# Kernel tuning notes

Hardware: AMD Instinct MI355X
Metric: run time of the kernel (lower is better)

The kernel has to match this reference:

```python
import jax, jax.numpy as jnp
import numpy as np

EPS = 1e-7  # keras.backend.epsilon()


def setup_inputs() -> dict:
    key = jax.random.key(0)
    kx, kw, ku = jax.random.split(key, 3)
    B, S, F = 16, 4096, 512
    x = jax.random.normal(kx, (B, S, F), dtype=jnp.float32)
    # glorot-uniform-scaled weights
    limW = np.sqrt(6.0 / (F + F)).astype(np.float32)
    W = jax.random.uniform(kw, (F, F), dtype=jnp.float32, minval=-limW, maxval=limW)
    b = jnp.zeros((F,), dtype=jnp.float32)
    limu = np.sqrt(6.0 / (F + 1)).astype(np.float32)
    u = jax.random.uniform(ku, (F,), dtype=jnp.float32, minval=-limu, maxval=limu)
    return {"x": x, "W": W, "b": b, "u": u}


def reference(x, W, b, u):
    # x: [B,S,F]  W: [F,F]  b: [F]  u: [F]
    h = jnp.tanh(jnp.einsum('bsf,fg->bsg', x, W) + b)   # [B,S,F]
    scores = jnp.einsum('bsf,f->bs', h, u)              # [B,S]
    e = jnp.exp(scores)
    # NOTE: faithful to the source, normalization is GLOBAL over all B*S scores
    a = e / (jnp.sum(e) + EPS)                          # [B,S]
    out = jnp.einsum('bsf,bs->bf', x, a)                # [B,F] weighted-sum pool over steps
    return out
```

## Files before the change

### kernel.cpp

```cpp
#include <hip/hip_runtime.h>
#include <stdint.h>

#define EPSV 1e-7f
#define FDIM 512
#define BK 64
#define NROWS 65536

typedef __bf16 bf16_t;
typedef bf16_t bf16x8 __attribute__((ext_vector_type(8)));
typedef unsigned short ushort8 __attribute__((ext_vector_type(8)));
typedef float f32x4 __attribute__((ext_vector_type(4)));

#define AS1 __attribute__((address_space(1)))
#define AS3 __attribute__((address_space(3)))

__device__ __forceinline__ unsigned short f2bf(float f) {
  union { float f; unsigned int u; } c; c.f = f;
  unsigned int u = c.u;
  unsigned int r = u + 0x7fffu + ((u >> 16) & 1u);
  return (unsigned short)(r >> 16);
}

__device__ __forceinline__ float fast_tanh(float x) {
  x = fminf(15.0f, fmaxf(-15.0f, x));
  float t = __expf(2.0f * x);
  return 1.0f - 2.0f * __builtin_amdgcn_rcpf(t + 1.0f);
}

__global__ void convert_W(const float* __restrict__ W, unsigned short* __restrict__ Wt) {
  __shared__ unsigned short tile[32][34];
  const int t = threadIdx.x;
  const int tx = t & 31, ty = t >> 5;
  const int bn = blockIdx.x & 15, bk = blockIdx.x >> 4;
  const int k0 = bk * 32, n0 = bn * 32;
#pragma unroll
  for (int i = 0; i < 4; ++i) {
    int r = ty + i * 8;
    tile[r][tx] = f2bf(W[(size_t)(k0 + r) * FDIM + n0 + tx]);
  }
  __syncthreads();
#pragma unroll
  for (int i = 0; i < 4; ++i) {
    int r = ty + i * 8;
    Wt[(size_t)(n0 + r) * FDIM + k0 + tx] = tile[tx][r];
  }
}

__global__ __launch_bounds__(256, 4) void gemm_score(
    const float* __restrict__ x, const unsigned short* __restrict__ Wt,
    const float* __restrict__ bvec, const float* __restrict__ uvec,
    float* __restrict__ spart) {
  __shared__ unsigned short sA[128 * BK];
  __shared__ unsigned short sB[128 * BK];
  __shared__ float score_s[128];
  __shared__ float ub_s[128], bb_s[128];

  const int t = threadIdx.x;
  const int lane = t & 63;
  const int w = t >> 6;
  const int wm = w & 1;
  const int wn = w >> 1;
  const int quad = lane >> 4;
  const int l15 = lane & 15;
  const int rt = blockIdx.x >> 2;
  const int nch = blockIdx.x & 3;
  const int m0 = rt * 128;
  const int col0 = nch * 128;

  if (t < 128) {
    score_s[t] = 0.0f;
    ub_s[t] = uvec[col0 + t];
    bb_s[t] = bvec[col0 + t];
  }

  f32x4 acc[4][4];
#pragma unroll
  for (int mi = 0; mi < 4; ++mi)
#pragma unroll
    for (int ni = 0; ni < 4; ++ni) acc[mi][ni] = (f32x4){0.f, 0.f, 0.f, 0.f};

  for (int kc = 0; kc < FDIM / BK; ++kc) {
    const int kbase = kc * BK;
#pragma unroll
    for (int p = 0; p < 4; ++p) {
      int slot = t + 256 * p;
      int row = slot >> 3;
      int j = (slot & 7) ^ (row & 7);
      const float* g = x + (size_t)(m0 + row) * FDIM + kbase + j * 8;
      float4 lo = *(const float4*)g;
      float4 hi = *(const float4*)(g + 4);
      ushort8 v;
      v[0] = f2bf(lo.x); v[1] = f2bf(lo.y); v[2] = f2bf(lo.z); v[3] = f2bf(lo.w);
      v[4] = f2bf(hi.x); v[5] = f2bf(hi.y); v[6] = f2bf(hi.z); v[7] = f2bf(hi.w);
      *(ushort8*)(void*)(sA + slot * 8) = v;
    }
#pragma unroll
    for (int i = 0; i < 4; ++i) {
      int nb = w * 32 + i * 8;
      int nl = nb + (lane >> 3);
      int j = (lane & 7) ^ (nl & 7);
      const unsigned short* g =
          Wt + (size_t)(col0 + nl) * FDIM + kbase + j * 8;
      unsigned short* l = (unsigned short*)(sB + nb * 64);
      __builtin_amdgcn_global_load_lds((AS1 void*)(g), (AS3 void*)(l), 16, 0, 0);
    }
    __syncthreads();
#pragma unroll
    for (int ks = 0; ks < 2; ++ks) {
      bf16x8 af[4], bfr[4];
#pragma unroll
      for (int mi = 0; mi < 4; ++mi) {
        int row = wm * 64 + mi * 16 + l15;
        int phys = (ks * 4 + quad) ^ (row & 7);
        af[mi] = *(const bf16x8*)(const void*)(sA + row * 64 + phys * 8);
      }
#pragma unroll
      for (int ni = 0; ni < 4; ++ni) {
        int row = wn * 64 + ni * 16 + l15;
        int phys = (ks * 4 + quad) ^ (row & 7);
        bfr[ni] = *(const bf16x8*)(const void*)(sB + row * 64 + phys * 8);
      }
#pragma unroll
      for (int mi = 0; mi < 4; ++mi)
#pragma unroll
        for (int ni = 0; ni < 4; ++ni)
          acc[mi][ni] = __builtin_amdgcn_mfma_f32_16x16x32_bf16(
              af[mi], bfr[ni], acc[mi][ni], 0, 0, 0);
    }
    __syncthreads();
  }

  float sc[4][4];
#pragma unroll
  for (int mi = 0; mi < 4; ++mi)
#pragma unroll
    for (int r = 0; r < 4; ++r) sc[mi][r] = 0.0f;
#pragma unroll
  for (int ni = 0; ni < 4; ++ni) {
    int cl = wn * 64 + ni * 16 + l15;
    float uu = ub_s[cl], bb = bb_s[cl];
#pragma unroll
    for (int mi = 0; mi < 4; ++mi)
#pragma unroll
      for (int r = 0; r < 4; ++r)
        sc[mi][r] += uu * fast_tanh(acc[mi][ni][r] + bb);
  }
#pragma unroll
  for (int mi = 0; mi < 4; ++mi)
#pragma unroll
    for (int r = 0; r < 4; ++r) {
      float v = sc[mi][r];
      v += __shfl_xor(v, 1); v += __shfl_xor(v, 2);
      v += __shfl_xor(v, 4); v += __shfl_xor(v, 8);
      if (l15 == 0)
        atomicAdd(&score_s[wm * 64 + mi * 16 + quad * 4 + r], v);
    }
  __syncthreads();
  if (t < 128) spart[(size_t)nch * NROWS + m0 + t] = score_s[t];
}

__global__ void score_exp(float* __restrict__ spart, float* __restrict__ sumE) {
  __shared__ float ws_[4];
  const int t = threadIdx.x;
  const int i = blockIdx.x * 256 + t;
  float s = spart[i] + spart[i + NROWS] + spart[i + 2 * NROWS] + spart[i + 3 * NROWS];
  float e = __expf(s);
  spart[i] = e;
  float v = e;
  v += __shfl_xor(v, 1);  v += __shfl_xor(v, 2);  v += __shfl_xor(v, 4);
  v += __shfl_xor(v, 8);  v += __shfl_xor(v, 16); v += __shfl_xor(v, 32);
  if ((t & 63) == 0) ws_[t >> 6] = v;
  __syncthreads();
  if (t == 0) atomicAdd(sumE, ws_[0] + ws_[1] + ws_[2] + ws_[3]);
}

__global__ __launch_bounds__(256) void pool_k(
    const float* __restrict__ x, const float* __restrict__ e,
    const float* __restrict__ sumE, float* __restrict__ out) {
  __shared__ float e_s[128];
  __shared__ float4 red[128];
  const int t = threadIdx.x;
  const int b = blockIdx.x >> 5, chunk = blockIdx.x & 31;
  const int g0 = b * 4096 + chunk * 128;
  if (t < 128) e_s[t] = e[g0 + t];
  __syncthreads();
  const int parity = t >> 7, f4 = t & 127;
  float ax = 0.f, ay = 0.f, az = 0.f, aw = 0.f;
  for (int r = 0; r < 64; ++r) {
    int row = r * 2 + parity;
    const float4 xv = *(const float4*)(x + (size_t)(g0 + row) * FDIM + f4 * 4);
    float wgt = e_s[row];
    ax += xv.x * wgt; ay += xv.y * wgt; az += xv.z * wgt; aw += xv.w * wgt;
  }
  if (parity) red[f4] = (float4){ax, ay, az, aw};
  __syncthreads();
  if (!parity) {
    float4 o = red[f4];
    float inv = 1.0f / (*sumE + EPSV);
    float* op = out + (size_t)b * FDIM + f4 * 4;
    atomicAdd(op + 0, (ax + o.x) * inv);
    atomicAdd(op + 1, (ay + o.y) * inv);
    atomicAdd(op + 2, (az + o.z) * inv);
    atomicAdd(op + 3, (aw + o.w) * inv);
  }
}

extern "C" void kernel_launch(void* const* d_in, const int* in_sizes, int n_in,
                              void* d_out, int out_size, void* d_ws, size_t ws_size,
                              hipStream_t stream) {
  (void)in_sizes; (void)n_in; (void)ws_size;
  const float* x = (const float*)d_in[0];
  const float* W = (const float*)d_in[1];
  const float* b = (const float*)d_in[2];
  const float* u = (const float*)d_in[3];
  float* out = (float*)d_out;

  unsigned short* Wt = (unsigned short*)d_ws;
  float* spart = (float*)((char*)d_ws + (size_t)FDIM * FDIM * sizeof(unsigned short));
  float* sumE = spart + 4 * NROWS;

  hipMemsetAsync(d_out, 0, (size_t)out_size * sizeof(float), stream);
  hipMemsetAsync(sumE, 0, sizeof(float), stream);

  convert_W<<<dim3(256), dim3(256), 0, stream>>>(W, Wt);
  gemm_score<<<dim3(2048), dim3(256), 0, stream>>>(x, Wt, b, u, spart);
  score_exp<<<dim3(NROWS / 256), dim3(256), 0, stream>>>(spart, sumE);
  pool_k<<<dim3(512), dim3(256), 0, stream>>>(x, spart, sumE, out);
}
```

Baseline: 277.0 us.

## Pre-convert x to bf16 once and reuse it for GEMM loads and pooling

Adds a kernel that converts all of x to bf16 in workspace. The GEMM then loads its A tiles straight into LDS with global_load_lds instead of converting fp32 to bf16 in every block, and the pooling reads the half-size bf16 copy. Pooling becomes per-block partial sums plus a separate reduce kernel, which removes the atomics and the output memset. The GEMM block order is also changed so the column chunk is the slowest-varying index. The cost is an extra 64MB write and read plus coarser pooling precision. The new path only runs when the workspace is large enough, otherwise the old path is used.

```diff
diff --git a/kernel.cpp b/kernel.cpp
--- a/kernel.cpp
+++ b/kernel.cpp
@@ -20,6 +20,10 @@
   unsigned int r = u + 0x7fffu + ((u >> 16) & 1u);
   return (unsigned short)(r >> 16);
 }
+__device__ __forceinline__ float bf2f(unsigned short s) {
+  union { unsigned int u; float f; } c; c.u = ((unsigned int)s) << 16;
+  return c.f;
+}
 
 __device__ __forceinline__ float fast_tanh(float x) {
   x = fminf(15.0f, fmaxf(-15.0f, x));
@@ -46,8 +50,21 @@
   }
 }
 
+__global__ __launch_bounds__(256) void convert_x(const float* __restrict__ x,
+                                                 unsigned short* __restrict__ xbf) {
+  size_t i = ((size_t)blockIdx.x * 256 + threadIdx.x) * 8;
+  float4 lo = *(const float4*)(x + i);
+  float4 hi = *(const float4*)(x + i + 4);
+  ushort8 v;
+  v[0] = f2bf(lo.x); v[1] = f2bf(lo.y); v[2] = f2bf(lo.z); v[3] = f2bf(lo.w);
+  v[4] = f2bf(hi.x); v[5] = f2bf(hi.y); v[6] = f2bf(hi.z); v[7] = f2bf(hi.w);
+  *(ushort8*)(xbf + i) = v;
+}
+
+template <bool ABF>
 __global__ __launch_bounds__(256, 4) void gemm_score(
-    const float* __restrict__ x, const unsigned short* __restrict__ Wt,
+    const float* __restrict__ x, const unsigned short* __restrict__ xbf,
+    const unsigned short* __restrict__ Wt,
     const float* __restrict__ bvec, const float* __restrict__ uvec,
     float* __restrict__ spart) {
   __shared__ unsigned short sA[128 * BK];
@@ -62,8 +79,8 @@
   const int wn = w >> 1;
   const int quad = lane >> 4;
   const int l15 = lane & 15;
-  const int rt = blockIdx.x >> 2;
-  const int nch = blockIdx.x & 3;
+  const int nch = blockIdx.x >> 9;
+  const int rt = blockIdx.x & 511;
   const int m0 = rt * 128;
   const int col0 = nch * 128;
 
@@ -81,18 +98,31 @@
 
   for (int kc = 0; kc < FDIM / BK; ++kc) {
     const int kbase = kc * BK;
-#pragma unroll
-    for (int p = 0; p < 4; ++p) {
-      int slot = t + 256 * p;
-      int row = slot >> 3;
-      int j = (slot & 7) ^ (row & 7);
-      const float* g = x + (size_t)(m0 + row) * FDIM + kbase + j * 8;
-      float4 lo = *(const float4*)g;
-      float4 hi = *(const float4*)(g + 4);
-      ushort8 v;
-      v[0] = f2bf(lo.x); v[1] = f2bf(lo.y); v[2] = f2bf(lo.z); v[3] = f2bf(lo.w);
-      v[4] = f2bf(hi.x); v[5] = f2bf(hi.y); v[6] = f2bf(hi.z); v[7] = f2bf(hi.w);
-      *(ushort8*)(void*)(sA + slot * 8) = v;
+    if constexpr (ABF) {
+#pragma unroll
+      for (int i = 0; i < 4; ++i) {
+        int rb = w * 32 + i * 8;
+        int rl = rb + (lane >> 3);
+        int j = (lane & 7) ^ (rl & 7);
+        const unsigned short* g =
+            xbf + (size_t)(m0 + rl) * FDIM + kbase + j * 8;
+        unsigned short* l = (unsigned short*)(sA + rb * 64);
+        __builtin_amdgcn_global_load_lds((AS1 void*)(g), (AS3 void*)(l), 16, 0, 0);
+      }
+    } else {
+#pragma unroll
+      for (int p = 0; p < 4; ++p) {
+        int slot = t + 256 * p;
+        int row = slot >> 3;
+        int j = (slot & 7) ^ (row & 7);
+        const float* g = x + (size_t)(m0 + row) * FDIM + kbase + j * 8;
+        float4 lo = *(const float4*)g;
+        float4 hi = *(const float4*)(g + 4);
+        ushort8 v;
+        v[0] = f2bf(lo.x); v[1] = f2bf(lo.y); v[2] = f2bf(lo.z); v[3] = f2bf(lo.w);
+        v[4] = f2bf(hi.x); v[5] = f2bf(hi.y); v[6] = f2bf(hi.z); v[7] = f2bf(hi.w);
+        *(ushort8*)(void*)(sA + slot * 8) = v;
+      }
     }
 #pragma unroll
     for (int i = 0; i < 4; ++i) {
@@ -174,6 +204,47 @@
   if (t == 0) atomicAdd(sumE, ws_[0] + ws_[1] + ws_[2] + ws_[3]);
 }
 
+__global__ __launch_bounds__(256, 8) void pool_part(
+    const unsigned short* __restrict__ xbf, const float* __restrict__ e,
+    float* __restrict__ ppool) {
+  __shared__ float e_s[32];
+  __shared__ float red[4][FDIM];
+  const int t = threadIdx.x;
+  const int c8 = t & 63, rg = t >> 6;
+  const int r0 = blockIdx.x * 32;
+  if (t < 32) e_s[t] = e[r0 + t];
+  __syncthreads();
+  float a[8];
+#pragma unroll
+  for (int j = 0; j < 8; ++j) a[j] = 0.0f;
+  for (int it = 0; it < 8; ++it) {
+    int row = rg * 8 + it;
+    ushort8 v = *(const ushort8*)(xbf + (size_t)(r0 + row) * FDIM + c8 * 8);
+    float wg = e_s[row];
+#pragma unroll
+    for (int j = 0; j < 8; ++j) a[j] += bf2f(v[j]) * wg;
+  }
+  *(float4*)&red[rg][c8 * 8]     = (float4){a[0], a[1], a[2], a[3]};
+  *(float4*)&red[rg][c8 * 8 + 4] = (float4){a[4], a[5], a[6], a[7]};
+  __syncthreads();
+  int c = t, c2 = t + 256;
+  float s0 = red[0][c] + red[1][c] + red[2][c] + red[3][c];
+  float s1 = red[0][c2] + red[1][c2] + red[2][c2] + red[3][c2];
+  ppool[(size_t)blockIdx.x * FDIM + c]  = s0;
+  ppool[(size_t)blockIdx.x * FDIM + c2] = s1;
+}
+
+__global__ __launch_bounds__(256) void pool_reduce(
+    const float* __restrict__ ppool, const float* __restrict__ sumE,
+    float* __restrict__ out) {
+  const int i = blockIdx.x * 256 + threadIdx.x;
+  const int b = i >> 9, f = i & 511;
+  float s = 0.0f;
+  const float* p = ppool + (size_t)b * 128 * FDIM + f;
+  for (int c = 0; c < 128; ++c) s += p[(size_t)c * FDIM];
+  out[i] = s / (*sumE + EPSV);
+}
+
 __global__ __launch_bounds__(256) void pool_k(
     const float* __restrict__ x, const float* __restrict__ e,
     const float* __restrict__ sumE, float* __restrict__ out) {
@@ -208,22 +279,35 @@
 extern "C" void kernel_launch(void* const* d_in, const int* in_sizes, int n_in,
                               void* d_out, int out_size, void* d_ws, size_t ws_size,
                               hipStream_t stream) {
-  (void)in_sizes; (void)n_in; (void)ws_size;
+  (void)in_sizes; (void)n_in;
   const float* x = (const float*)d_in[0];
   const float* W = (const float*)d_in[1];
   const float* b = (const float*)d_in[2];
   const float* u = (const float*)d_in[3];
   float* out = (float*)d_out;
 
-  unsigned short* Wt = (unsigned short*)d_ws;
-  float* spart = (float*)((char*)d_ws + (size_t)FDIM * FDIM * sizeof(unsigned short));
-  float* sumE = spart + 4 * NROWS;
-
-  hipMemsetAsync(d_out, 0, (size_t)out_size * sizeof(float), stream);
+  char* p = (char*)d_ws;
+  unsigned short* Wt = (unsigned short*)p;            p += (size_t)FDIM * FDIM * 2;
+  float* spart = (float*)p;                           p += (size_t)4 * NROWS * 4;
+  float* sumE = (float*)p;                            p += 256;
+  float* ppool = (float*)p;                           p += (size_t)2048 * FDIM * 4;
+  unsigned short* xbf = (unsigned short*)p;           p += (size_t)NROWS * FDIM * 2;
+  const size_t need = (size_t)(p - (char*)d_ws);
+  const bool big = ws_size >= need;
+
   hipMemsetAsync(sumE, 0, sizeof(float), stream);
-
   convert_W<<<dim3(256), dim3(256), 0, stream>>>(W, Wt);
-  gemm_score<<<dim3(2048), dim3(256), 0, stream>>>(x, Wt, b, u, spart);
-  score_exp<<<dim3(NROWS / 256), dim3(256), 0, stream>>>(spart, sumE);
-  pool_k<<<dim3(512), dim3(256), 0, stream>>>(x, spart, sumE, out);
-}
+
+  if (big) {
+    convert_x<<<dim3(NROWS * FDIM / (256 * 8)), dim3(256), 0, stream>>>(x, xbf);
+    gemm_score<true><<<dim3(2048), dim3(256), 0, stream>>>(x, xbf, Wt, b, u, spart);
+    score_exp<<<dim3(NROWS / 256), dim3(256), 0, stream>>>(spart, sumE);
+    pool_part<<<dim3(2048), dim3(256), 0, stream>>>(xbf, spart, ppool);
+    pool_reduce<<<dim3(32), dim3(256), 0, stream>>>(ppool, sumE, out);
+  } else {
+    hipMemsetAsync(d_out, 0, (size_t)out_size * sizeof(float), stream);
+    gemm_score<false><<<dim3(2048), dim3(256), 0, stream>>>(x, xbf, Wt, b, u, spart);
+    score_exp<<<dim3(NROWS / 256), dim3(256), 0, stream>>>(spart, sumE);
+    pool_k<<<dim3(512), dim3(256), 0, stream>>>(x, spart, sumE, out);
+  }
+}
```

New measurement: 274.6 us. About the same (-0.9%).
